# Kernel tuning notes

Hardware: AMD Instinct MI355X
Metric: run time of the kernel (lower is better)

Reference implementation:

```python
import jax, jax.numpy as jnp
import numpy as np

N_POOL, DIM_EMB, DIM_HID, FIRST_DIM = 4, 128, 128, 134
N_NODES_TOT, N_GRAPHS = 250000, 256
EPS = 1e-16  # PyG softmax eps


def setup_inputs() -> dict:
    key = jax.random.key(0)
    ks = jax.random.split(key, 20)
    inp = {
        "x": jax.random.normal(ks[0], (N_NODES_TOT, FIRST_DIM), jnp.float32),
        "batch": jnp.sort(jax.random.randint(ks[1], (N_NODES_TOT,), 0, N_GRAPHS)),
        "n_nodes": jax.random.uniform(ks[2], (N_GRAPHS, 1), jnp.float32),
        "Omegas": jax.random.uniform(ks[3], (N_GRAPHS, 1), jnp.float32),
        "Phis": jax.random.uniform(ks[4], (N_GRAPHS, 1), jnp.float32),
        "Lambdas": jax.random.uniform(ks[5], (N_GRAPHS, 1), jnp.float32),
        "Omegas_norm": jax.random.uniform(ks[6], (N_GRAPHS, 1), jnp.float32),
        "Phis_norm": jax.random.uniform(ks[7], (N_GRAPHS, 1), jnp.float32),
        "Lambdas_norm": jax.random.uniform(ks[8], (N_GRAPHS, 1), jnp.float32),
    }
    s1 = 1.0 / np.sqrt(FIRST_DIM)
    s2 = 1.0 / np.sqrt(DIM_HID)
    # stacked params for the n_pool GlobalAttention modules
    inp["gate_w1"] = jax.random.uniform(ks[9], (N_POOL, FIRST_DIM, DIM_HID), jnp.float32, -s1, s1)
    inp["gate_b1"] = jax.random.uniform(ks[10], (N_POOL, DIM_HID), jnp.float32, -s1, s1)
    inp["gate_w2"] = jax.random.uniform(ks[11], (N_POOL, DIM_HID), jnp.float32, -s2, s2)
    inp["gate_b2"] = jax.random.uniform(ks[12], (N_POOL,), jnp.float32, -s2, s2)
    inp["nn_w1"] = jax.random.uniform(ks[13], (N_POOL, FIRST_DIM, DIM_HID), jnp.float32, -s1, s1)
    inp["nn_b1"] = jax.random.uniform(ks[14], (N_POOL, DIM_HID), jnp.float32, -s1, s1)
    inp["nn_w2"] = jax.random.uniform(ks[15], (N_POOL, DIM_HID, DIM_EMB), jnp.float32, -s2, s2)
    inp["nn_b2"] = jax.random.uniform(ks[16], (N_POOL, DIM_EMB), jnp.float32, -s2, s2)
    return inp


def reference(x, batch, n_nodes, Omegas, Phis, Lambdas, Omegas_norm, Phis_norm,
              Lambdas_norm, gate_w1, gate_b1, gate_w2, gate_b2, nn_w1, nn_b1,
              nn_w2, nn_b2):
    B = n_nodes.shape[0]
    # gate scores: per-node scalar per pool head -> [N, K]
    g1 = jax.nn.relu(jnp.einsum("nf,kfh->nkh", x, gate_w1) + gate_b1)
    scores = jnp.einsum("nkh,kh->nk", g1, gate_w2) + gate_b2
    # batch-segmented softmax (stable, PyG style)
    m = jax.ops.segment_max(scores, batch, num_segments=B)          # [B, K]
    e = jnp.exp(scores - m[batch])                                  # [N, K]
    denom = jax.ops.segment_sum(e, batch, num_segments=B)[batch] + EPS
    gate = e / denom                                                # [N, K]
    # node transform per pool -> [N, K, D]
    h1 = jax.nn.relu(jnp.einsum("nf,kfh->nkh", x, nn_w1) + nn_b1)
    v = jnp.einsum("nkh,khd->nkd", h1, nn_w2) + nn_b2
    # gated segment-sum pooling -> [B, K, D], concat pools -> [B, K*D]
    pooled = jax.ops.segment_sum(gate[..., None] * v, batch, num_segments=B)
    ctx_emb = pooled.reshape(B, N_POOL * DIM_EMB)
    return jnp.concatenate(
        [ctx_emb, n_nodes, Omegas, Phis, Lambdas, Omegas_norm, Phis_norm,
         Lambdas_norm], axis=1)
```

## Files before the change

kernel.cpp:

```cpp
#include <hip/hip_runtime.h>
#include <math.h>

#define N_NODES 250000
#define F_DIM   134
#define H_DIM   128
#define K_POOL  4
#define B_GR    256
#define EPSF    1e-16f
#define OUT_W   (K_POOL * H_DIM + 7)

#define BM      128
#define BK      32
#define KP      160
#define KSTEPS  5
#define GMAX    16
#define NBLK    ((N_NODES + BM - 1) / BM)
#define N_PAD   (NBLK * BM)

#define SZ_X       (N_PAD * KP * 2)
#define SZ_W       (K_POOL * H_DIM * KP * 2)
#define OFF_XH     0
#define OFF_XL     (OFF_XH + SZ_X)
#define OFF_WHG    (OFF_XL + SZ_X)
#define OFF_WLG    (OFF_WHG + SZ_W)
#define OFF_WHN    (OFF_WLG + SZ_W)
#define OFF_WLN    (OFF_WHN + SZ_W)
#define OFF_SCORES (OFF_WLN + SZ_W)
#define OFF_SEG    (OFF_SCORES + N_NODES * 16)
#define OFF_MAX    (OFF_SEG + 2048)
#define OFF_DEN    (OFF_MAX + 4096)
#define OFF_POOL   (OFF_DEN + 4096)

typedef __attribute__((ext_vector_type(8))) short bf16x8;
typedef __attribute__((ext_vector_type(4))) float f32x4;

__device__ __forceinline__ ushort f2bf(float f) {
    union { float f; unsigned u; } v; v.f = f;
    const unsigned u = v.u;
    return (ushort)((u + 0x7FFFu + ((u >> 16) & 1u)) >> 16);
}
__device__ __forceinline__ float bf2f(ushort h) {
    union { unsigned u; float f; } v; v.u = ((unsigned)h) << 16; return v.f;
}
__device__ __forceinline__ int swz(int row, int kg) {
    return ((row << 6) + (kg << 4)) ^ ((row & 7) << 4);
}

__launch_bounds__(256)
__global__ void cvt_x_kernel(const float* __restrict__ x,
                             ushort* __restrict__ xh, ushort* __restrict__ xl)
{
    const int idx = (blockIdx.x * 256 + threadIdx.x) * 4;
    if (idx >= N_PAD * KP) return;
    const int row = idx / KP;
    const int col = idx - row * KP;
    float v[4] = {0.f, 0.f, 0.f, 0.f};
    if (row < N_NODES) {
        const float* xr = x + row * F_DIM + col;
        if (col + 4 <= F_DIM) {
            float2 a = *(const float2*)(xr);
            float2 b = *(const float2*)(xr + 2);
            v[0] = a.x; v[1] = a.y; v[2] = b.x; v[3] = b.y;
        } else if (col < F_DIM) {
            float2 a = *(const float2*)(xr);
            v[0] = a.x; v[1] = a.y;
        }
    }
    ushort4 h, l;
    h.x = f2bf(v[0]); l.x = f2bf(v[0] - bf2f(h.x));
    h.y = f2bf(v[1]); l.y = f2bf(v[1] - bf2f(h.y));
    h.z = f2bf(v[2]); l.z = f2bf(v[2] - bf2f(h.z));
    h.w = f2bf(v[3]); l.w = f2bf(v[3] - bf2f(h.w));
    *(ushort4*)(xh + idx) = h;
    *(ushort4*)(xl + idx) = l;
}

__launch_bounds__(256)
__global__ void cvt_w_kernel(const float* __restrict__ wg, const float* __restrict__ wn,
                             ushort* __restrict__ whg, ushort* __restrict__ wlg,
                             ushort* __restrict__ whn, ushort* __restrict__ wln)
{
    const int idx = blockIdx.x * 256 + threadIdx.x;
    if (idx >= K_POOL * H_DIM * KP) return;
    const int k   = idx % KP;
    const int pc  = idx / KP;
    const int col = pc & 127, p = pc >> 7;
    const float* src = blockIdx.y ? wn : wg;
    const float v = (k < F_DIM) ? src[(p * F_DIM + k) * H_DIM + col] : 0.f;
    const ushort h = f2bf(v);
    const ushort lo = f2bf(v - bf2f(h));
    if (blockIdx.y) { whn[idx] = h; wln[idx] = lo; }
    else            { whg[idx] = h; wlg[idx] = lo; }
}

__device__ __forceinline__ void mm_stage(const ushort* __restrict__ Ahs,
                                         const ushort* __restrict__ Als,
                                         const ushort* __restrict__ Bhs,
                                         const ushort* __restrict__ Bls,
                                         int kbeg, int t,
                                         short* Ah, short* Al, short* Bh, short* Bl)
{
    const int row  = t >> 1;
    const int half = t & 1;
    const int base = row * KP + kbeg + half * 16;
    const int off0 = swz(row, half * 2) >> 1;
    const int off1 = swz(row, half * 2 + 1) >> 1;
    *(bf16x8*)(Ah + off0) = *(const bf16x8*)(Ahs + base);
    *(bf16x8*)(Ah + off1) = *(const bf16x8*)(Ahs + base + 8);
    *(bf16x8*)(Al + off0) = *(const bf16x8*)(Als + base);
    *(bf16x8*)(Al + off1) = *(const bf16x8*)(Als + base + 8);
    *(bf16x8*)(Bh + off0) = *(const bf16x8*)(Bhs + base);
    *(bf16x8*)(Bh + off1) = *(const bf16x8*)(Bhs + base + 8);
    *(bf16x8*)(Bl + off0) = *(const bf16x8*)(Bls + base);
    *(bf16x8*)(Bl + off1) = *(const bf16x8*)(Bls + base + 8);
}

__device__ __forceinline__ void mm_compute(int t, const short* Ah, const short* Al,
                                           const short* Bh, const short* Bl,
                                           f32x4 acc[2][8])
{
    const int lane = t & 63, wv = t >> 6;
    bf16x8 ah[2], al[2];
#pragma unroll
    for (int r = 0; r < 2; ++r) {
        const int rowA = wv * 32 + r * 16 + (lane & 15);
        const int off  = swz(rowA, lane >> 4) >> 1;
        ah[r] = *(const bf16x8*)(Ah + off);
        al[r] = *(const bf16x8*)(Al + off);
    }
#pragma unroll
    for (int c = 0; c < 8; ++c) {
        const int rowB = c * 16 + (lane & 15);
        const int off  = swz(rowB, lane >> 4) >> 1;
        const bf16x8 bh = *(const bf16x8*)(Bh + off);
        const bf16x8 bl = *(const bf16x8*)(Bl + off);
#pragma unroll
        for (int r = 0; r < 2; ++r) {
            acc[r][c] = __builtin_amdgcn_mfma_f32_16x16x32_bf16(ah[r], bh, acc[r][c], 0, 0, 0);
            acc[r][c] = __builtin_amdgcn_mfma_f32_16x16x32_bf16(ah[r], bl, acc[r][c], 0, 0, 0);
            acc[r][c] = __builtin_amdgcn_mfma_f32_16x16x32_bf16(al[r], bh, acc[r][c], 0, 0, 0);
        }
    }
}

__global__ void seg_kernel(const int* __restrict__ batch, int* __restrict__ seg) {
    int b = blockIdx.x * blockDim.x + threadIdx.x;
    if (b > B_GR) return;
    int lo = 0, hi = N_NODES;
    while (lo < hi) {
        int mid = (lo + hi) >> 1;
        if (batch[mid] < b) lo = mid + 1; else hi = mid;
    }
    seg[b] = lo;
}

__launch_bounds__(256, 2)
__global__ void gate_kernel(const ushort* __restrict__ xh, const ushort* __restrict__ xl,
                            const ushort* __restrict__ wh, const ushort* __restrict__ wl,
                            const float* __restrict__ b1,
                            const float* __restrict__ w2,
                            const float* __restrict__ b2,
                            float* __restrict__ scores)
{
    __shared__ short Ah[4096], Al[4096], Bh[4096], Bl[4096];
    const int k = blockIdx.y, m0 = blockIdx.x * BM, t = threadIdx.x;
    const ushort* Ahs = xh + (long)m0 * KP;
    const ushort* Als = xl + (long)m0 * KP;
    const ushort* Bhs = wh + k * H_DIM * KP;
    const ushort* Bls = wl + k * H_DIM * KP;

    f32x4 acc[2][8];
    const f32x4 z = {0.f, 0.f, 0.f, 0.f};
#pragma unroll
    for (int r = 0; r < 2; ++r)
#pragma unroll
        for (int c = 0; c < 8; ++c) acc[r][c] = z;

    for (int ks = 0; ks < KSTEPS; ++ks) {
        __syncthreads();
        mm_stage(Ahs, Als, Bhs, Bls, ks * BK, t, Ah, Al, Bh, Bl);
        __syncthreads();
        mm_compute(t, Ah, Al, Bh, Bl, acc);
    }

    const int lane = t & 63, wv = t >> 6;
    float b1v[8], w2v[8];
#pragma unroll
    for (int c = 0; c < 8; ++c) {
        const int col = c * 16 + (lane & 15);
        b1v[c] = b1[k * H_DIM + col];
        w2v[c] = w2[k * H_DIM + col];
    }
    const float b2v = b2[k];
#pragma unroll
    for (int r = 0; r < 2; ++r)
#pragma unroll
        for (int q = 0; q < 4; ++q) {
            float s = 0.f;
#pragma unroll
            for (int c = 0; c < 8; ++c)
                s = fmaf(fmaxf(acc[r][c][q] + b1v[c], 0.f), w2v[c], s);
            s += __shfl_xor(s, 1); s += __shfl_xor(s, 2);
            s += __shfl_xor(s, 4); s += __shfl_xor(s, 8);
            if ((lane & 15) == 0) {
                const int m = m0 + wv * 32 + r * 16 + (lane >> 4) * 4 + q;
                if (m < N_NODES) scores[m * 4 + k] = s + b2v;
            }
        }
}

__launch_bounds__(256)
__global__ void stats_kernel(const float* __restrict__ scores,
                             const int* __restrict__ seg,
                             float* __restrict__ maxv,
                             float* __restrict__ denom,
                             float* __restrict__ pooled)
{
    const int g = blockIdx.x;
    const int t = threadIdx.x;
    const int s = seg[g], e = seg[g + 1];
    const float4* sc4 = (const float4*)scores;

    float mx[4] = {-INFINITY, -INFINITY, -INFINITY, -INFINITY};
    for (int n = s + t; n < e; n += 256) {
        float4 v = sc4[n];
        mx[0] = fmaxf(mx[0], v.x); mx[1] = fmaxf(mx[1], v.y);
        mx[2] = fmaxf(mx[2], v.z); mx[3] = fmaxf(mx[3], v.w);
    }
#pragma unroll
    for (int c = 0; c < 4; ++c)
        for (int off = 32; off; off >>= 1)
            mx[c] = fmaxf(mx[c], __shfl_down(mx[c], off));

    __shared__ float redbuf[4][4];
    __shared__ float bmax[4];
    const int wid = t >> 6, lane = t & 63;
    if (lane == 0)
#pragma unroll
        for (int c = 0; c < 4; ++c) redbuf[wid][c] = mx[c];
    __syncthreads();
    if (t == 0)
#pragma unroll
        for (int c = 0; c < 4; ++c) {
            float m = redbuf[0][c];
            m = fmaxf(m, redbuf[1][c]); m = fmaxf(m, redbuf[2][c]); m = fmaxf(m, redbuf[3][c]);
            bmax[c] = m;
        }
    __syncthreads();
    const float m0v = bmax[0], m1v = bmax[1], m2v = bmax[2], m3v = bmax[3];

    float sm[4] = {0.f, 0.f, 0.f, 0.f};
    for (int n = s + t; n < e; n += 256) {
        float4 v = sc4[n];
        sm[0] += expf(v.x - m0v); sm[1] += expf(v.y - m1v);
        sm[2] += expf(v.z - m2v); sm[3] += expf(v.w - m3v);
    }
#pragma unroll
    for (int c = 0; c < 4; ++c)
        for (int off = 32; off; off >>= 1)
            sm[c] += __shfl_down(sm[c], off);
    __syncthreads();
    if (lane == 0)
#pragma unroll
        for (int c = 0; c < 4; ++c) redbuf[wid][c] = sm[c];
    __syncthreads();
    if (t == 0)
#pragma unroll
        for (int c = 0; c < 4; ++c) {
            maxv[g * 4 + c]  = bmax[c];
            denom[g * 4 + c] = redbuf[0][c] + redbuf[1][c] + redbuf[2][c] + redbuf[3][c] + EPSF;
        }
    pooled[g * 512 + t]       = 0.f;
    pooled[g * 512 + 256 + t] = 0.f;
}

__launch_bounds__(256, 2)
__global__ void pool_kernel(const ushort* __restrict__ xh, const ushort* __restrict__ xl,
                            const ushort* __restrict__ wh, const ushort* __restrict__ wl,
                            const int* __restrict__ batch,
                            const float* __restrict__ b1,
                            const float* __restrict__ scores,
                            const float* __restrict__ maxv,
                            const float* __restrict__ denom,
                            float* __restrict__ pooled)
{
    __shared__ short Ah[4096], Al[4096], Bh[4096], Bl[4096];
    __shared__ float lds_pool[GMAX][H_DIM];
    const int k = blockIdx.y, m0 = blockIdx.x * BM, t = threadIdx.x;
    const ushort* Ahs = xh + (long)m0 * KP;
    const ushort* Als = xl + (long)m0 * KP;
    const ushort* Bhs = wh + k * H_DIM * KP;
    const ushort* Bls = wl + k * H_DIM * KP;

    for (int idx = t; idx < GMAX * H_DIM; idx += 256)
        ((float*)lds_pool)[idx] = 0.f;

    f32x4 acc[2][8];
    const f32x4 z = {0.f, 0.f, 0.f, 0.f};
#pragma unroll
    for (int r = 0; r < 2; ++r)
#pragma unroll
        for (int c = 0; c < 8; ++c) acc[r][c] = z;

    for (int ks = 0; ks < KSTEPS; ++ks) {
        __syncthreads();
        mm_stage(Ahs, Als, Bhs, Bls, ks * BK, t, Ah, Al, Bh, Bl);
        __syncthreads();
        mm_compute(t, Ah, Al, Bh, Bl, acc);
    }

    const int lane = t & 63, wv = t >> 6;
    const int gfirst0 = batch[m0];
    float b1v[8];
#pragma unroll
    for (int c = 0; c < 8; ++c)
        b1v[c] = b1[k * H_DIM + c * 16 + (lane & 15)];

#pragma unroll
    for (int r = 0; r < 2; ++r) {
        const int mrow = m0 + wv * 32 + r * 16;
        if (mrow >= N_NODES) continue;
        const int mhi   = (mrow + 15 < N_NODES) ? mrow + 15 : N_NODES - 1;
        const int ga    = batch[mrow];
        const bool unif = (batch[mhi] == ga) && (mrow + 15 < N_NODES);
        if (unif) {
            const float mxv = maxv[ga * 4 + k];
            const float den = denom[ga * 4 + k];
            float gates[4];
#pragma unroll
            for (int q = 0; q < 4; ++q) {
                const int m = mrow + (lane >> 4) * 4 + q;
                gates[q] = expf(scores[m * 4 + k] - mxv) / den;
            }
            const int lg = ga - gfirst0;
#pragma unroll
            for (int c = 0; c < 8; ++c) {
                float p = 0.f;
#pragma unroll
                for (int q = 0; q < 4; ++q)
                    p = fmaf(gates[q], fmaxf(acc[r][c][q] + b1v[c], 0.f), p);
                p += __shfl_xor(p, 16);
                p += __shfl_xor(p, 32);
                if (lane < 16) {
                    if (lg < GMAX) atomicAdd(&lds_pool[lg][c * 16 + lane], p);
                    else atomicAdd(&pooled[(ga * K_POOL + k) * H_DIM + c * 16 + lane], p);
                }
            }
        } else {
#pragma unroll
            for (int q = 0; q < 4; ++q) {
                const int m = mrow + (lane >> 4) * 4 + q;
                const bool val = m < N_NODES;
                int g = ga; float gate = 0.f;
                if (val) {
                    g = batch[m];
                    gate = expf(scores[m * 4 + k] - maxv[g * 4 + k]) / denom[g * 4 + k];
                }
                const int lg = g - gfirst0;
#pragma unroll
                for (int c = 0; c < 8; ++c) {
                    const float v = gate * fmaxf(acc[r][c][q] + b1v[c], 0.f);
                    if (val && v != 0.f) {
                        if (lg < GMAX) atomicAdd(&lds_pool[lg][c * 16 + (lane & 15)], v);
                        else atomicAdd(&pooled[(g * K_POOL + k) * H_DIM + c * 16 + (lane & 15)], v);
                    }
                }
            }
        }
    }

    __syncthreads();
    {
        const int mlast = (m0 + BM - 1 < N_NODES) ? m0 + BM - 1 : N_NODES - 1;
        int span = batch[mlast] - gfirst0 + 1;
        if (span > GMAX) span = GMAX;
        for (int idx = t; idx < span * H_DIM; idx += 256) {
            const float v = ((const float*)lds_pool)[idx];
            if (v != 0.f)
                atomicAdd(&pooled[((gfirst0 + (idx >> 7)) * K_POOL + k) * H_DIM + (idx & 127)], v);
        }
    }
}

__launch_bounds__(128)
__global__ void out_kernel(const float* __restrict__ pooled,
                           const float* __restrict__ w2,
                           const float* __restrict__ b2,
                           const float* __restrict__ denom,
                           const float* __restrict__ s0, const float* __restrict__ s1,
                           const float* __restrict__ s2, const float* __restrict__ s3,
                           const float* __restrict__ s4, const float* __restrict__ s5,
                           const float* __restrict__ s6,
                           float* __restrict__ out)
{
    const int g = blockIdx.x;
    const int t = threadIdx.x;
    __shared__ float ps[H_DIM];
    float* orow = out + g * OUT_W;

    for (int k = 0; k < K_POOL; ++k) {
        __syncthreads();
        ps[t] = pooled[(g * K_POOL + k) * H_DIM + t];
        __syncthreads();
        const float den = denom[g * 4 + k];
        const float gs  = (den - EPSF) / den;
        float a = b2[k * H_DIM + t] * gs;
        const float* wkt = w2 + (k * H_DIM) * H_DIM + t;
#pragma unroll 4
        for (int h = 0; h < H_DIM; ++h)
            a = fmaf(ps[h], wkt[h * H_DIM], a);
        orow[k * H_DIM + t] = a;
    }
    if (t < 7) {
        const float* sp;
        switch (t) {
            case 0: sp = s0; break; case 1: sp = s1; break; case 2: sp = s2; break;
            case 3: sp = s3; break; case 4: sp = s4; break; case 5: sp = s5; break;
            default: sp = s6; break;
        }
        orow[K_POOL * H_DIM + t] = sp[g];
    }
}

extern "C" void kernel_launch(void* const* d_in, const int* in_sizes, int n_in,
                              void* d_out, int out_size, void* d_ws, size_t ws_size,
                              hipStream_t stream) {
    const float* x     = (const float*)d_in[0];
    const int*   batch = (const int*)d_in[1];
    const float* n_nodes = (const float*)d_in[2];
    const float* Omegas  = (const float*)d_in[3];
    const float* Phis    = (const float*)d_in[4];
    const float* Lambdas = (const float*)d_in[5];
    const float* Omn     = (const float*)d_in[6];
    const float* Phn     = (const float*)d_in[7];
    const float* Lan     = (const float*)d_in[8];
    const float* gw1 = (const float*)d_in[9];
    const float* gb1 = (const float*)d_in[10];
    const float* gw2 = (const float*)d_in[11];
    const float* gb2 = (const float*)d_in[12];
    const float* nw1 = (const float*)d_in[13];
    const float* nb1 = (const float*)d_in[14];
    const float* nw2 = (const float*)d_in[15];
    const float* nb2 = (const float*)d_in[16];

    char* ws = (char*)d_ws;
    ushort* xh  = (ushort*)(ws + OFF_XH);
    ushort* xl  = (ushort*)(ws + OFF_XL);
    ushort* whg = (ushort*)(ws + OFF_WHG);
    ushort* wlg = (ushort*)(ws + OFF_WLG);
    ushort* whn = (ushort*)(ws + OFF_WHN);
    ushort* wln = (ushort*)(ws + OFF_WLN);
    float* scores = (float*)(ws + OFF_SCORES);
    int*   seg    = (int*)(ws + OFF_SEG);
    float* maxv   = (float*)(ws + OFF_MAX);
    float* denom  = (float*)(ws + OFF_DEN);
    float* pooled = (float*)(ws + OFF_POOL);
    float* out    = (float*)d_out;

    cvt_x_kernel<<<(N_PAD * KP / 4 + 255) / 256, 256, 0, stream>>>(x, xh, xl);
    dim3 wgrid((K_POOL * H_DIM * KP + 255) / 256, 2);
    cvt_w_kernel<<<wgrid, 256, 0, stream>>>(gw1, nw1, whg, wlg, whn, wln);
    seg_kernel<<<2, 256, 0, stream>>>(batch, seg);

    dim3 gemm_grid(NBLK, K_POOL);
    gate_kernel<<<gemm_grid, 256, 0, stream>>>(xh, xl, whg, wlg, gb1, gw2, gb2, scores);
    stats_kernel<<<B_GR, 256, 0, stream>>>(scores, seg, maxv, denom, pooled);
    pool_kernel<<<gemm_grid, 256, 0, stream>>>(xh, xl, whn, wln, batch, nb1,
                                               scores, maxv, denom, pooled);
    out_kernel<<<B_GR, 128, 0, stream>>>(pooled, nw2, nb2, denom,
                                         n_nodes, Omegas, Phis, Lambdas, Omn, Phn, Lan, out);
}
```

Before: 743.7 us.

## Loop over pool heads inside gate and pool GEMM blocks instead of grid dimension

The gate and pool kernels now handle all four pool heads in one block by looping over k, instead of using a second grid dimension. The aim is to raise L2 reuse of each X tile and to combine the LDS pool partials for all heads before the global atomics, which lowers atomic traffic. The LDS pool buffer becomes [GMAX][K][H] with GMAX cut to 4 so shared memory stays bounded. The cost is four times fewer blocks, each running serially longer, and more global atomics when a 128-row tile spans more than four graphs (about 977 nodes per graph makes that rare).

```diff
diff --git a/kernel.cpp b/kernel.cpp
--- a/kernel.cpp
+++ b/kernel.cpp
@@ -13,7 +13,7 @@
 #define BK      32
 #define KP      160
 #define KSTEPS  5
-#define GMAX    16
+#define GMAX    4
 #define NBLK    ((N_NODES + BM - 1) / BM)
 #define N_PAD   (NBLK * BM)
 
@@ -163,50 +163,53 @@
                             float* __restrict__ scores)
 {
     __shared__ short Ah[4096], Al[4096], Bh[4096], Bl[4096];
-    const int k = blockIdx.y, m0 = blockIdx.x * BM, t = threadIdx.x;
+    const int m0 = blockIdx.x * BM, t = threadIdx.x;
+    const int lane = t & 63, wv = t >> 6;
     const ushort* Ahs = xh + (long)m0 * KP;
     const ushort* Als = xl + (long)m0 * KP;
-    const ushort* Bhs = wh + k * H_DIM * KP;
-    const ushort* Bls = wl + k * H_DIM * KP;
-
-    f32x4 acc[2][8];
-    const f32x4 z = {0.f, 0.f, 0.f, 0.f};
-#pragma unroll
-    for (int r = 0; r < 2; ++r)
-#pragma unroll
-        for (int c = 0; c < 8; ++c) acc[r][c] = z;
-
-    for (int ks = 0; ks < KSTEPS; ++ks) {
-        __syncthreads();
-        mm_stage(Ahs, Als, Bhs, Bls, ks * BK, t, Ah, Al, Bh, Bl);
-        __syncthreads();
-        mm_compute(t, Ah, Al, Bh, Bl, acc);
-    }
-
-    const int lane = t & 63, wv = t >> 6;
-    float b1v[8], w2v[8];
-#pragma unroll
-    for (int c = 0; c < 8; ++c) {
-        const int col = c * 16 + (lane & 15);
-        b1v[c] = b1[k * H_DIM + col];
-        w2v[c] = w2[k * H_DIM + col];
-    }
-    const float b2v = b2[k];
-#pragma unroll
-    for (int r = 0; r < 2; ++r)
-#pragma unroll
-        for (int q = 0; q < 4; ++q) {
-            float s = 0.f;
-#pragma unroll
-            for (int c = 0; c < 8; ++c)
-                s = fmaf(fmaxf(acc[r][c][q] + b1v[c], 0.f), w2v[c], s);
-            s += __shfl_xor(s, 1); s += __shfl_xor(s, 2);
-            s += __shfl_xor(s, 4); s += __shfl_xor(s, 8);
-            if ((lane & 15) == 0) {
-                const int m = m0 + wv * 32 + r * 16 + (lane >> 4) * 4 + q;
-                if (m < N_NODES) scores[m * 4 + k] = s + b2v;
+
+    for (int k = 0; k < K_POOL; ++k) {
+        const ushort* Bhs = wh + k * H_DIM * KP;
+        const ushort* Bls = wl + k * H_DIM * KP;
+
+        f32x4 acc[2][8];
+        const f32x4 z = {0.f, 0.f, 0.f, 0.f};
+#pragma unroll
+        for (int r = 0; r < 2; ++r)
+#pragma unroll
+            for (int c = 0; c < 8; ++c) acc[r][c] = z;
+
+        for (int ks = 0; ks < KSTEPS; ++ks) {
+            __syncthreads();
+            mm_stage(Ahs, Als, Bhs, Bls, ks * BK, t, Ah, Al, Bh, Bl);
+            __syncthreads();
+            mm_compute(t, Ah, Al, Bh, Bl, acc);
+        }
+
+        float b1v[8], w2v[8];
+#pragma unroll
+        for (int c = 0; c < 8; ++c) {
+            const int col = c * 16 + (lane & 15);
+            b1v[c] = b1[k * H_DIM + col];
+            w2v[c] = w2[k * H_DIM + col];
+        }
+        const float b2v = b2[k];
+#pragma unroll
+        for (int r = 0; r < 2; ++r)
+#pragma unroll
+            for (int q = 0; q < 4; ++q) {
+                float s = 0.f;
+#pragma unroll
+                for (int c = 0; c < 8; ++c)
+                    s = fmaf(fmaxf(acc[r][c][q] + b1v[c], 0.f), w2v[c], s);
+                s += __shfl_xor(s, 1); s += __shfl_xor(s, 2);
+                s += __shfl_xor(s, 4); s += __shfl_xor(s, 8);
+                if ((lane & 15) == 0) {
+                    const int m = m0 + wv * 32 + r * 16 + (lane >> 4) * 4 + q;
+                    if (m < N_NODES) scores[m * 4 + k] = s + b2v;
+                }
             }
-        }
+    }
 }
 
 __launch_bounds__(256)
@@ -285,84 +288,88 @@
                             float* __restrict__ pooled)
 {
     __shared__ short Ah[4096], Al[4096], Bh[4096], Bl[4096];
-    __shared__ float lds_pool[GMAX][H_DIM];
-    const int k = blockIdx.y, m0 = blockIdx.x * BM, t = threadIdx.x;
+    __shared__ float lds_pool[GMAX][K_POOL][H_DIM];
+    const int m0 = blockIdx.x * BM, t = threadIdx.x;
+    const int lane = t & 63, wv = t >> 6;
     const ushort* Ahs = xh + (long)m0 * KP;
     const ushort* Als = xl + (long)m0 * KP;
-    const ushort* Bhs = wh + k * H_DIM * KP;
-    const ushort* Bls = wl + k * H_DIM * KP;
-
-    for (int idx = t; idx < GMAX * H_DIM; idx += 256)
+
+    for (int idx = t; idx < GMAX * K_POOL * H_DIM; idx += 256)
         ((float*)lds_pool)[idx] = 0.f;
 
-    f32x4 acc[2][8];
-    const f32x4 z = {0.f, 0.f, 0.f, 0.f};
-#pragma unroll
-    for (int r = 0; r < 2; ++r)
-#pragma unroll
-        for (int c = 0; c < 8; ++c) acc[r][c] = z;
-
-    for (int ks = 0; ks < KSTEPS; ++ks) {
-        __syncthreads();
-        mm_stage(Ahs, Als, Bhs, Bls, ks * BK, t, Ah, Al, Bh, Bl);
-        __syncthreads();
-        mm_compute(t, Ah, Al, Bh, Bl, acc);
-    }
-
-    const int lane = t & 63, wv = t >> 6;
     const int gfirst0 = batch[m0];
-    float b1v[8];
-#pragma unroll
-    for (int c = 0; c < 8; ++c)
-        b1v[c] = b1[k * H_DIM + c * 16 + (lane & 15)];
-
-#pragma unroll
-    for (int r = 0; r < 2; ++r) {
-        const int mrow = m0 + wv * 32 + r * 16;
-        if (mrow >= N_NODES) continue;
-        const int mhi   = (mrow + 15 < N_NODES) ? mrow + 15 : N_NODES - 1;
-        const int ga    = batch[mrow];
-        const bool unif = (batch[mhi] == ga) && (mrow + 15 < N_NODES);
-        if (unif) {
-            const float mxv = maxv[ga * 4 + k];
-            const float den = denom[ga * 4 + k];
-            float gates[4];
-#pragma unroll
-            for (int q = 0; q < 4; ++q) {
-                const int m = mrow + (lane >> 4) * 4 + q;
-                gates[q] = expf(scores[m * 4 + k] - mxv) / den;
-            }
-            const int lg = ga - gfirst0;
-#pragma unroll
-            for (int c = 0; c < 8; ++c) {
-                float p = 0.f;
-#pragma unroll
-                for (int q = 0; q < 4; ++q)
-                    p = fmaf(gates[q], fmaxf(acc[r][c][q] + b1v[c], 0.f), p);
-                p += __shfl_xor(p, 16);
-                p += __shfl_xor(p, 32);
-                if (lane < 16) {
-                    if (lg < GMAX) atomicAdd(&lds_pool[lg][c * 16 + lane], p);
-                    else atomicAdd(&pooled[(ga * K_POOL + k) * H_DIM + c * 16 + lane], p);
+
+    for (int k = 0; k < K_POOL; ++k) {
+        const ushort* Bhs = wh + k * H_DIM * KP;
+        const ushort* Bls = wl + k * H_DIM * KP;
+
+        f32x4 acc[2][8];
+        const f32x4 z = {0.f, 0.f, 0.f, 0.f};
+#pragma unroll
+        for (int r = 0; r < 2; ++r)
+#pragma unroll
+            for (int c = 0; c < 8; ++c) acc[r][c] = z;
+
+        for (int ks = 0; ks < KSTEPS; ++ks) {
+            __syncthreads();
+            mm_stage(Ahs, Als, Bhs, Bls, ks * BK, t, Ah, Al, Bh, Bl);
+            __syncthreads();
+            mm_compute(t, Ah, Al, Bh, Bl, acc);
+        }
+
+        float b1v[8];
+#pragma unroll
+        for (int c = 0; c < 8; ++c)
+            b1v[c] = b1[k * H_DIM + c * 16 + (lane & 15)];
+
+#pragma unroll
+        for (int r = 0; r < 2; ++r) {
+            const int mrow = m0 + wv * 32 + r * 16;
+            if (mrow >= N_NODES) continue;
+            const int mhi   = (mrow + 15 < N_NODES) ? mrow + 15 : N_NODES - 1;
+            const int ga    = batch[mrow];
+            const bool unif = (batch[mhi] == ga) && (mrow + 15 < N_NODES);
+            if (unif) {
+                const float mxv = maxv[ga * 4 + k];
+                const float den = denom[ga * 4 + k];
+                float gates[4];
+#pragma unroll
+                for (int q = 0; q < 4; ++q) {
+                    const int m = mrow + (lane >> 4) * 4 + q;
+                    gates[q] = expf(scores[m * 4 + k] - mxv) / den;
                 }
-            }
-        } else {
-#pragma unroll
-            for (int q = 0; q < 4; ++q) {
-                const int m = mrow + (lane >> 4) * 4 + q;
-                const bool val = m < N_NODES;
-                int g = ga; float gate = 0.f;
-                if (val) {
-                    g = batch[m];
-                    gate = expf(scores[m * 4 + k] - maxv[g * 4 + k]) / denom[g * 4 + k];
+                const int lg = ga - gfirst0;
+#pragma unroll
+                for (int c = 0; c < 8; ++c) {
+                    float p = 0.f;
+#pragma unroll
+                    for (int q = 0; q < 4; ++q)
+                        p = fmaf(gates[q], fmaxf(acc[r][c][q] + b1v[c], 0.f), p);
+                    p += __shfl_xor(p, 16);
+                    p += __shfl_xor(p, 32);
+                    if (lane < 16) {
+                        if (lg < GMAX) atomicAdd(&lds_pool[lg][k][c * 16 + lane], p);
+                        else atomicAdd(&pooled[(ga * K_POOL + k) * H_DIM + c * 16 + lane], p);
+                    }
                 }
-                const int lg = g - gfirst0;
-#pragma unroll
-                for (int c = 0; c < 8; ++c) {
-                    const float v = gate * fmaxf(acc[r][c][q] + b1v[c], 0.f);
-                    if (val && v != 0.f) {
-                        if (lg < GMAX) atomicAdd(&lds_pool[lg][c * 16 + (lane & 15)], v);
-                        else atomicAdd(&pooled[(g * K_POOL + k) * H_DIM + c * 16 + (lane & 15)], v);
+            } else {
+#pragma unroll
+                for (int q = 0; q < 4; ++q) {
+                    const int m = mrow + (lane >> 4) * 4 + q;
+                    const bool val = m < N_NODES;
+                    int g = ga; float gate = 0.f;
+                    if (val) {
+                        g = batch[m];
+                        gate = expf(scores[m * 4 + k] - maxv[g * 4 + k]) / denom[g * 4 + k];
+                    }
+                    const int lg = g - gfirst0;
+#pragma unroll
+                    for (int c = 0; c < 8; ++c) {
+                        const float v = gate * fmaxf(acc[r][c][q] + b1v[c], 0.f);
+                        if (val && v != 0.f) {
+                            if (lg < GMAX) atomicAdd(&lds_pool[lg][k][c * 16 + (lane & 15)], v);
+                            else atomicAdd(&pooled[(g * K_POOL + k) * H_DIM + c * 16 + (lane & 15)], v);
+                        }
                     }
                 }
             }
@@ -374,10 +381,13 @@
         const int mlast = (m0 + BM - 1 < N_NODES) ? m0 + BM - 1 : N_NODES - 1;
         int span = batch[mlast] - gfirst0 + 1;
         if (span > GMAX) span = GMAX;
-        for (int idx = t; idx < span * H_DIM; idx += 256) {
+        for (int idx = t; idx < span * K_POOL * H_DIM; idx += 256) {
             const float v = ((const float*)lds_pool)[idx];
-            if (v != 0.f)
-                atomicAdd(&pooled[((gfirst0 + (idx >> 7)) * K_POOL + k) * H_DIM + (idx & 127)], v);
+            if (v != 0.f) {
+                const int lg  = idx >> 9;
+                const int rem = idx & 511;
+                atomicAdd(&pooled[(gfirst0 + lg) * 512 + rem], v);
+            }
         }
     }
 }
@@ -462,11 +472,10 @@
     cvt_w_kernel<<<wgrid, 256, 0, stream>>>(gw1, nw1, whg, wlg, whn, wln);
     seg_kernel<<<2, 256, 0, stream>>>(batch, seg);
 
-    dim3 gemm_grid(NBLK, K_POOL);
-    gate_kernel<<<gemm_grid, 256, 0, stream>>>(xh, xl, whg, wlg, gb1, gw2, gb2, scores);
+    gate_kernel<<<NBLK, 256, 0, stream>>>(xh, xl, whg, wlg, gb1, gw2, gb2, scores);
     stats_kernel<<<B_GR, 256, 0, stream>>>(scores, seg, maxv, denom, pooled);
-    pool_kernel<<<gemm_grid, 256, 0, stream>>>(xh, xl, whn, wln, batch, nb1,
-                                               scores, maxv, denom, pooled);
+    pool_kernel<<<NBLK, 256, 0, stream>>>(xh, xl, whn, wln, batch, nb1,
+                                          scores, maxv, denom, pooled);
     out_kernel<<<B_GR, 128, 0, stream>>>(pooled, nw2, nb2, denom,
                                          n_nodes, Omegas, Phis, Lambdas, Omn, Phn, Lan, out);
 }
```

Measured after the change: 707.3 us. 1.05x faster.
